# Performance work log

Hardware: AMD Instinct MI355X
Metric: run time of the kernel (lower is better)

## Reference

```python
import jax, jax.numpy as jnp
import numpy as np

# shift search range (matches init_kwargs)
MIN_SX, MAX_SX = -4, 4
MIN_SY, MAX_SY = -4, 4
B, C, H, W = 4, 3, 512, 512


def _shift(x, sx, sy):
    """torch.roll on dims (1,2) of a [C,H,W] tensor, zeroing wrapped rows/cols.

    Equivalent to AutomatedShiftFix.shift: positive sx zeros rows [:sx],
    negative sx zeros rows [sx:]; same for sy on the W axis.
    """
    h, w = x.shape[1], x.shape[2]
    shifted = jnp.roll(x, (sx, sy), axis=(1, 2))
    i = jnp.arange(h)[:, None]   # [H,1]
    j = jnp.arange(w)[None, :]   # [1,W]
    mask_h = jnp.where(sx >= 0, i >= sx, i < h + sx)
    mask_w = jnp.where(sy >= 0, j >= sy, j < w + sy)
    mask = (mask_h & mask_w).astype(x.dtype)  # [H,W]
    return shifted * mask[None]


def _all_shifts():
    sx = jnp.arange(MIN_SX, MAX_SX + 1)
    sy = jnp.arange(MIN_SY, MAX_SY + 1)
    # outer loop over shift_x, inner over shift_y -> 'ij' matches torch ordering
    return jnp.stack(jnp.meshgrid(sx, sy, indexing="ij"), axis=-1).reshape(-1, 2)  # [Ns,2]


def setup_inputs() -> dict:
    key = jax.random.key(0)
    k1, k2 = jax.random.split(key)
    x_ref = jax.random.normal(k1, (B, C, H, W), dtype=jnp.float32)
    x = jax.random.normal(k2, (B, C, H, W), dtype=jnp.float32)
    return {"x_ref": x_ref, "x": x}


def reference(x_ref, x):
    shifts = _all_shifts()  # [Ns,2] int32

    def sims_one(xr, xi):  # xr, xi: [C,H,W]
        # similarity for every candidate shift: sum over (C,H,W) of shifted*ref
        return jax.vmap(lambda s: jnp.sum(_shift(xi, s[0], s[1]) * xr))(shifts)  # [Ns]

    sims = jax.vmap(sims_one)(x_ref, x)          # [B, Ns]
    best = jnp.argmax(sims, axis=1)              # [B]
    best_shifts = shifts[best]                   # [B, 2]
    out = jax.vmap(lambda xi, s: _shift(xi, s[0], s[1]))(x, best_shifts)  # [B,C,H,W]
    return out, best_shifts
```

## Files before the change

### kernel.cpp

```cpp
#include <hip/hip_runtime.h>

#define BB 4
#define CC 3
#define HH 512
#define WW 512
#define NS 81
#define IMG (HH * WW)
#define CHW (CC * IMG)
#define STRIP 16
#define NSTRIPS (HH / STRIP)
#define NBLK (BB * CC * NSTRIPS)
#define SLOTS (CC * NSTRIPS)

__device__ double g_part[(size_t)BB * NS * SLOTS];
__device__ int    g_best[BB];

#define C4(v, i) ((i) == 0 ? (v).x : (i) == 1 ? (v).y : (i) == 2 ? (v).z : (v).w)

__global__ __launch_bounds__(576) void k_sims(const float* __restrict__ xref,
                                              const float* __restrict__ x) {
    int bid   = blockIdx.x;
    int strip = bid % NSTRIPS;
    int bc    = bid / NSTRIPS;
    int b     = bc / CC;
    const float* xp = x    + (size_t)bc * IMG;
    const float* rp = xref + (size_t)bc * IMG;
    int tid  = threadIdx.x;
    int lane = tid & 63;
    int sxi  = tid >> 6;
    int j0   = lane << 3;
    int sx   = sxi - 4;
    int ip0  = strip * STRIP;

    float acc[9];
#pragma unroll
    for (int s = 0; s < 9; ++s) acc[s] = 0.f;

#pragma unroll
    for (int rr = 0; rr < STRIP; ++rr) {
        int ip = ip0 + rr;
        int ii = ip + sx;
        if ((unsigned)ii >= HH) continue;

        const float* xrow = xp + ip * WW + j0;
        const float* rrow = rp + ii * WW + j0;
        float4 xa = *(const float4*)(xrow);
        float4 xb = *(const float4*)(xrow + 4);
        float4 ra = *(const float4*)(rrow);
        float4 rb = *(const float4*)(rrow + 4);

        float p0 = __shfl_up(rb.x, 1, 64);
        float p1 = __shfl_up(rb.y, 1, 64);
        float p2 = __shfl_up(rb.z, 1, 64);
        float p3 = __shfl_up(rb.w, 1, 64);
        if (lane == 0) { p0 = p1 = p2 = p3 = 0.f; }
        float n0 = __shfl_down(ra.x, 1, 64);
        float n1 = __shfl_down(ra.y, 1, 64);
        float n2 = __shfl_down(ra.z, 1, 64);
        float n3 = __shfl_down(ra.w, 1, 64);
        if (lane == 63) { n0 = n1 = n2 = n3 = 0.f; }

#define P4(i) ((i) == 0 ? p0 : (i) == 1 ? p1 : (i) == 2 ? p2 : p3)
#define N4(i) ((i) == 0 ? n0 : (i) == 1 ? n1 : (i) == 2 ? n2 : n3)
#pragma unroll
        for (int syi = 0; syi < 9; ++syi) {
#pragma unroll
            for (int k = 0; k < 8; ++k) {
                int i = k + syi;
                float wv = (i < 4)  ? P4(i)
                         : (i < 8)  ? C4(ra, i - 4)
                         : (i < 12) ? C4(rb, i - 8)
                         :            N4(i - 12);
                float xv = (k < 4) ? C4(xa, k) : C4(xb, k - 4);
                acc[syi] += xv * wv;
            }
        }
#undef P4
#undef N4
    }

    int cs = (bc % CC) * NSTRIPS + strip;
#pragma unroll
    for (int s = 0; s < 9; ++s) {
        float v = acc[s];
        for (int off = 32; off; off >>= 1) v += __shfl_down(v, off, 64);
        if (lane == 0)
            g_part[((size_t)b * NS + sxi * 9 + s) * SLOTS + cs] = (double)v;
    }
}

__global__ __launch_bounds__(128) void k_reduce(float* __restrict__ outTail) {
    int b = blockIdx.x;
    int t = threadIdx.x;
    __shared__ double vals[NS];
    if (t < NS) {
        const double* p = g_part + ((size_t)b * NS + t) * SLOTS;
        double s = 0.0;
        for (int i = 0; i < SLOTS; ++i) s += p[i];
        vals[t] = s;
    }
    __syncthreads();
    if (t == 0) {
        int best = 0;
        double bv = vals[0];
        for (int i = 1; i < NS; ++i)
            if (vals[i] > bv) { bv = vals[i]; best = i; }
        g_best[b] = best;
        outTail[b * 2]     = (float)(best / 9 - 4);
        outTail[b * 2 + 1] = (float)(best % 9 - 4);
    }
}

__global__ __launch_bounds__(256) void k_apply(const float* __restrict__ x,
                                               float* __restrict__ out) {
    int blk = blockIdx.x;
    int bc  = blk >> 8;
    int tid = threadIdx.x;
    int b   = bc / CC;

    int bi = g_best[b];
    int sx = bi / 9 - 4;
    int sy = bi % 9 - 4;

    int row = ((blk & 255) << 1) + (tid >> 7);
    int j0  = (tid & 127) << 2;
    int is  = row - sx;
    float4 v = make_float4(0.f, 0.f, 0.f, 0.f);
    if ((unsigned)is < HH) {
        const float* src = x + (size_t)bc * IMG + is * WW;
        int js0 = j0 - sy;
        if (js0 >= 0 && js0 + 3 < WW) {
            v = *(const float4*)(src + js0);
        } else {
            float* vv = (float*)&v;
#pragma unroll
            for (int k = 0; k < 4; ++k) {
                int js = js0 + k;
                if ((unsigned)js < WW) vv[k] = src[js];
            }
        }
    }
    *(float4*)(out + (size_t)bc * IMG + row * WW + j0) = v;
}

extern "C" void kernel_launch(void* const* d_in, const int* in_sizes, int n_in,
                              void* d_out, int out_size, void* d_ws, size_t ws_size,
                              hipStream_t stream) {
    const float* xref = (const float*)d_in[0];
    const float* x    = (const float*)d_in[1];
    float* out = (float*)d_out;
    (void)d_ws; (void)ws_size;

    k_sims<<<NBLK, 576, 0, stream>>>(xref, x);
    k_reduce<<<BB, 128, 0, stream>>>(out + (size_t)BB * CHW);

    int applyBlocks = (BB * CC * HH) / 2;
    k_apply<<<applyBlocks, 256, 0, stream>>>(x, out);
}
```

Measured before the change: 96.51 us.

## Halve strip size, swizzle blocks, load neighbors directly, split reduce accumulators

Each k_sims block now covers 8 rows instead of 16, so twice as many blocks run, and the kernel declares a minimum occupancy hint of 4 blocks. Block indices are remapped to interleave work across the grid. The neighbour reference values are now read with extra float4 global loads instead of cross-lane shuffles. The reduce kernel sums with two accumulators to shorten its dependency chain, at the cost of summing the many more partial slots the smaller strips create.

```diff
diff --git a/kernel.cpp b/kernel.cpp
--- a/kernel.cpp
+++ b/kernel.cpp
@@ -7,7 +7,7 @@
 #define NS 81
 #define IMG (HH * WW)
 #define CHW (CC * IMG)
-#define STRIP 16
+#define STRIP 8
 #define NSTRIPS (HH / STRIP)
 #define NBLK (BB * CC * NSTRIPS)
 #define SLOTS (CC * NSTRIPS)
@@ -17,9 +17,10 @@
 
 #define C4(v, i) ((i) == 0 ? (v).x : (i) == 1 ? (v).y : (i) == 2 ? (v).z : (v).w)
 
-__global__ __launch_bounds__(576) void k_sims(const float* __restrict__ xref,
-                                              const float* __restrict__ x) {
-    int bid   = blockIdx.x;
+__global__ __launch_bounds__(576, 4) void k_sims(const float* __restrict__ xref,
+                                                 const float* __restrict__ x) {
+    int raw   = blockIdx.x;
+    int bid   = (raw & 7) * (NBLK / 8) + (raw >> 3);
     int strip = bid % NSTRIPS;
     int bc    = bid / NSTRIPS;
     int b     = bc / CC;
@@ -46,37 +47,29 @@
         const float* rrow = rp + ii * WW + j0;
         float4 xa = *(const float4*)(xrow);
         float4 xb = *(const float4*)(xrow + 4);
+
+        const float4* pp = (const float4*)(rrow + (lane == 0  ? 0 : -4));
+        const float4* np = (const float4*)(rrow + (lane == 63 ? 0 :  8));
+        float4 pv = *pp;
         float4 ra = *(const float4*)(rrow);
         float4 rb = *(const float4*)(rrow + 4);
+        float4 nv = *np;
+        if (lane == 0)  pv = make_float4(0.f, 0.f, 0.f, 0.f);
+        if (lane == 63) nv = make_float4(0.f, 0.f, 0.f, 0.f);
 
-        float p0 = __shfl_up(rb.x, 1, 64);
-        float p1 = __shfl_up(rb.y, 1, 64);
-        float p2 = __shfl_up(rb.z, 1, 64);
-        float p3 = __shfl_up(rb.w, 1, 64);
-        if (lane == 0) { p0 = p1 = p2 = p3 = 0.f; }
-        float n0 = __shfl_down(ra.x, 1, 64);
-        float n1 = __shfl_down(ra.y, 1, 64);
-        float n2 = __shfl_down(ra.z, 1, 64);
-        float n3 = __shfl_down(ra.w, 1, 64);
-        if (lane == 63) { n0 = n1 = n2 = n3 = 0.f; }
-
-#define P4(i) ((i) == 0 ? p0 : (i) == 1 ? p1 : (i) == 2 ? p2 : p3)
-#define N4(i) ((i) == 0 ? n0 : (i) == 1 ? n1 : (i) == 2 ? n2 : n3)
 #pragma unroll
         for (int syi = 0; syi < 9; ++syi) {
 #pragma unroll
             for (int k = 0; k < 8; ++k) {
                 int i = k + syi;
-                float wv = (i < 4)  ? P4(i)
+                float wv = (i < 4)  ? C4(pv, i)
                          : (i < 8)  ? C4(ra, i - 4)
                          : (i < 12) ? C4(rb, i - 8)
-                         :            N4(i - 12);
+                         :            C4(nv, i - 12);
                 float xv = (k < 4) ? C4(xa, k) : C4(xb, k - 4);
                 acc[syi] += xv * wv;
             }
         }
-#undef P4
-#undef N4
     }
 
     int cs = (bc % CC) * NSTRIPS + strip;
@@ -95,9 +88,9 @@
     __shared__ double vals[NS];
     if (t < NS) {
         const double* p = g_part + ((size_t)b * NS + t) * SLOTS;
-        double s = 0.0;
-        for (int i = 0; i < SLOTS; ++i) s += p[i];
-        vals[t] = s;
+        double s0 = 0.0, s1 = 0.0;
+        for (int i = 0; i < SLOTS; i += 2) { s0 += p[i]; s1 += p[i + 1]; }
+        vals[t] = s0 + s1;
     }
     __syncthreads();
     if (t == 0) {
```

Measured after the change: 101.7 us. 5.4% more time.
